# Kernel optimization log

Measured on AMD Instinct MI355X. Metric: run time of the kernel, lower is better.

The kernel has to match this reference:

```python
import jax, jax.numpy as jnp
import numpy as np

B, T, C = 2, 2048, 2048
N_HEAD, N_KV_HEAD = 16, 4
HEAD_DIM = C // N_HEAD  # 128
EPS = 1e-6


def rms_norm(x):
    # no learned scale, normalize over head_dim (last axis)
    return x * jax.lax.rsqrt(jnp.mean(jnp.square(x), axis=-1, keepdims=True) + EPS)


def apply_rotary_emb(x, cos, sin):
    # x: [B, T, H, D]; cos/sin: [T, D/2]  (rotate-half RoPE)
    x1, x2 = jnp.split(x, 2, axis=-1)
    c = cos[None, :, None, :]
    s = sin[None, :, None, :]
    return jnp.concatenate([x1 * c - x2 * s, x1 * s + x2 * c], axis=-1)


def setup_inputs() -> dict:
    key = jax.random.key(0)
    ks = jax.random.split(key, 6)
    x = jax.random.normal(ks[0], (B, T, C), dtype=jnp.float32)
    # real rotary tables: theta = 10000^{-2i/D}
    inv_freq = 1.0 / (10000.0 ** (jnp.arange(0, HEAD_DIM, 2, dtype=jnp.float32) / HEAD_DIM))
    angles = jnp.arange(T, dtype=jnp.float32)[:, None] * inv_freq[None, :]  # [T, D/2]
    cos, sin = jnp.cos(angles), jnp.sin(angles)
    std = 0.02
    Wq = jax.random.normal(ks[1], (C, N_HEAD * HEAD_DIM), dtype=jnp.float32) * std
    Wk = jax.random.normal(ks[2], (C, N_KV_HEAD * HEAD_DIM), dtype=jnp.float32) * std
    Wv = jax.random.normal(ks[3], (C, N_KV_HEAD * HEAD_DIM), dtype=jnp.float32) * std
    Wp = jax.random.normal(ks[4], (C, C), dtype=jnp.float32) * std
    return {"x": x, "cos": cos, "sin": sin, "Wq": Wq, "Wk": Wk, "Wv": Wv, "Wp": Wp}


def reference(x, cos, sin, Wq, Wk, Wv, Wp):
    Bx, Tx, Cx = x.shape
    q = (x @ Wq).reshape(Bx, Tx, N_HEAD, HEAD_DIM)
    k = (x @ Wk).reshape(Bx, Tx, N_KV_HEAD, HEAD_DIM)
    v = (x @ Wv).reshape(Bx, Tx, N_KV_HEAD, HEAD_DIM)
    q = rms_norm(apply_rotary_emb(q, cos, sin))
    k = rms_norm(apply_rotary_emb(k, cos, sin))
    # module scales q by 1/sqrt(D) AND nn.dot_product_attention scales again
    q = q * (1.0 / jnp.sqrt(HEAD_DIM))
    # GQA head repeat
    n_rep = N_HEAD // N_KV_HEAD
    k = jnp.repeat(k, n_rep, axis=2)  # [B, T, H, D]
    v = jnp.repeat(v, n_rep, axis=2)
    scores = jnp.einsum("bthd,bshd->bhts", q, k) / jnp.sqrt(jnp.asarray(HEAD_DIM, x.dtype))
    causal = jnp.tril(jnp.ones((Tx, Tx), dtype=bool))  # key <= query
    scores = jnp.where(causal[None, None, :, :], scores, jnp.finfo(scores.dtype).min)
    probs = jax.nn.softmax(scores, axis=-1)
    y = jnp.einsum("bhts,bshd->bthd", probs, v).reshape(Bx, Tx, Cx)
    return y @ Wp
```

## Files before the change

### kernel.cpp

```cpp
#include <hip/hip_runtime.h>
#include <hip/hip_bf16.h>
#include <math.h>

#define B_  2
#define T_  2048
#define C_  2048
#define NH_ 16
#define NKV_ 4
#define HD_ 128
#define NREP_ (NH_/NKV_)

#define QKVLD 3072
#define KOFF  2048
#define VOFF  2560

typedef __bf16 bf16x8 __attribute__((ext_vector_type(8)));
typedef float  f32x4  __attribute__((ext_vector_type(4)));

__device__ inline void gload_lds16(const void* g, void* l) {
    __builtin_amdgcn_global_load_lds((const __attribute__((address_space(1))) void*)g,
                                     (__attribute__((address_space(3))) void*)l, 16, 0, 0);
}

__global__ __launch_bounds__(256) void cast_bf16(const float* __restrict__ src,
                                                 __bf16* __restrict__ dst)
{
    size_t i = ((size_t)blockIdx.x * 256 + threadIdx.x) * 8;
    float4 a = *(const float4*)&src[i];
    float4 b = *(const float4*)&src[i + 4];
    union { __bf16 h[8]; uint4 u; } pk;
    pk.h[0] = (__bf16)a.x; pk.h[1] = (__bf16)a.y; pk.h[2] = (__bf16)a.z; pk.h[3] = (__bf16)a.w;
    pk.h[4] = (__bf16)b.x; pk.h[5] = (__bf16)b.y; pk.h[6] = (__bf16)b.z; pk.h[7] = (__bf16)b.w;
    *(uint4*)&dst[i] = pk.u;
}

__global__ __launch_bounds__(256) void wtrans(const float* __restrict__ src,
                                              __bf16* __restrict__ dst, int ncols)
{
    __shared__ float tl[32][33];
    int n0 = blockIdx.x * 32;
    int k0 = blockIdx.y * 32;
    int tid = threadIdx.x;
    int r  = tid >> 3;
    int c4 = (tid & 7) * 4;
    float4 v = *(const float4*)&src[(size_t)(k0 + r) * ncols + n0 + c4];
    tl[r][c4] = v.x; tl[r][c4 + 1] = v.y; tl[r][c4 + 2] = v.z; tl[r][c4 + 3] = v.w;
    __syncthreads();
    union { __bf16 h[4]; uint2 u; } pk;
#pragma unroll
    for (int j = 0; j < 4; ++j) pk.h[j] = (__bf16)tl[c4 + j][r];
    *(uint2*)&dst[(size_t)(n0 + r) * 2048 + k0 + c4] = pk.u;
}

template<typename TOUT>
__global__ __launch_bounds__(256) void gemm_bt(const __bf16* __restrict__ A,
                                               const __bf16* __restrict__ Bt,
                                               TOUT* __restrict__ C,
                                               int M, int N, int K, int ldc)
{
    __shared__ __bf16 As[128 * 32];
    __shared__ __bf16 Bs[128 * 32];

    const int tid  = threadIdx.x;
    const int wv   = tid >> 6;
    const int lane = tid & 63;
    const int grp  = lane >> 4;
    const int id16 = lane & 15;
    const int wr   = wv >> 1;
    const int wc   = wv & 1;

    const int row0 = blockIdx.y * 128;
    const int col0 = blockIdx.x * 128;

    const int sm = tid >> 2;
    const int sk = (tid & 3) << 3;

    const __bf16* ga0 = A  + (size_t)(row0 + sm) * K + sk;
    const __bf16* ga1 = A  + (size_t)(row0 + 64 + sm) * K + sk;
    const __bf16* gb0 = Bt + (size_t)(col0 + sm) * K + sk;
    const __bf16* gb1 = Bt + (size_t)(col0 + 64 + sm) * K + sk;

    __bf16* lA0 = As + (wv << 9);
    __bf16* lA1 = As + 2048 + (wv << 9);
    __bf16* lB0 = Bs + (wv << 9);
    __bf16* lB1 = Bs + 2048 + (wv << 9);

    f32x4 acc[4][4];
    const f32x4 fz = {0.f, 0.f, 0.f, 0.f};
#pragma unroll
    for (int i = 0; i < 4; ++i)
#pragma unroll
        for (int j = 0; j < 4; ++j) acc[i][j] = fz;

    for (int k0 = 0; k0 < K; k0 += 32) {
        gload_lds16(ga0 + k0, lA0);
        gload_lds16(ga1 + k0, lA1);
        gload_lds16(gb0 + k0, lB0);
        gload_lds16(gb1 + k0, lB1);
        asm volatile("s_waitcnt vmcnt(0)" ::: "memory");
        __syncthreads();

        bf16x8 af[4], bfr[4];
#pragma unroll
        for (int i = 0; i < 4; ++i)
            af[i] = *(const bf16x8*)&As[((wr << 6) + (i << 4) + id16) * 32 + (grp << 3)];
#pragma unroll
        for (int j = 0; j < 4; ++j)
            bfr[j] = *(const bf16x8*)&Bs[((wc << 6) + (j << 4) + id16) * 32 + (grp << 3)];
#pragma unroll
        for (int i = 0; i < 4; ++i)
#pragma unroll
            for (int j = 0; j < 4; ++j)
                acc[i][j] = __builtin_amdgcn_mfma_f32_16x16x32_bf16(af[i], bfr[j], acc[i][j], 0, 0, 0);
        __syncthreads();
    }

#pragma unroll
    for (int i = 0; i < 4; ++i) {
        int gr = row0 + (wr << 6) + (i << 4) + (grp << 2);
#pragma unroll
        for (int j = 0; j < 4; ++j) {
            int gc = col0 + (wc << 6) + (j << 4) + id16;
#pragma unroll
            for (int r = 0; r < 4; ++r) {
                if constexpr (sizeof(TOUT) == 4)
                    C[(size_t)(gr + r) * ldc + gc] = acc[i][j][r];
                else
                    C[(size_t)(gr + r) * ldc + gc] = (TOUT)acc[i][j][r];
            }
        }
    }
}

__global__ __launch_bounds__(256) void rope_rms_b(__bf16* __restrict__ base,
                                                  const float* __restrict__ cosb,
                                                  const float* __restrict__ sinb,
                                                  int nheads, float scale)
{
    int wid  = blockIdx.x * 4 + (threadIdx.x >> 6);
    int lane = threadIdx.x & 63;
    int bt = wid / nheads;
    int hd = wid % nheads;
    int t  = bt % T_;

    __bf16* p = base + (size_t)bt * QKVLD + hd * HD_;
    float c = cosb[t * 64 + lane];
    float s = sinb[t * 64 + lane];
    float x1 = (float)p[lane];
    float x2 = (float)p[lane + 64];
    float r1 = x1 * c - x2 * s;
    float r2 = x1 * s + x2 * c;
    float ss = r1 * r1 + r2 * r2;
#pragma unroll
    for (int off = 32; off; off >>= 1) ss += __shfl_xor(ss, off, 64);
    float inv = rsqrtf(ss * (1.f / 128.f) + 1e-6f) * scale;
    p[lane]      = (__bf16)(r1 * inv);
    p[lane + 64] = (__bf16)(r2 * inv);
}

__global__ __launch_bounds__(256) void vtrans(const __bf16* __restrict__ qkv,
                                              __bf16* __restrict__ vt)
{
    __shared__ __bf16 tl[32][HD_ + 8];
    int bx  = blockIdx.x;
    int st  = bx & 63;
    int bkv = bx >> 6;
    int b = bkv >> 2, kv = bkv & 3;
    int s0 = st << 5;
    int tid = threadIdx.x;
    {
        int s = tid >> 3;
        int d = (tid & 7) << 4;
        const __bf16* src = qkv + (size_t)(b * T_ + s0 + s) * QKVLD + VOFF + kv * HD_ + d;
        *(bf16x8*)&tl[s][d]     = *(const bf16x8*)src;
        *(bf16x8*)&tl[s][d + 8] = *(const bf16x8*)(src + 8);
    }
    __syncthreads();
    {
        int d  = tid >> 1;
        int sh = (tid & 1) << 4;
        __bf16 tmp[16];
#pragma unroll
        for (int j = 0; j < 16; ++j) tmp[j] = tl[sh + j][d];
        __bf16* dst = vt + ((size_t)(b * NKV_ + kv) * HD_ + d) * T_ + s0 + sh;
        *(bf16x8*)dst       = *(bf16x8*)&tmp[0];
        *(bf16x8*)(dst + 8) = *(bf16x8*)&tmp[8];
    }
}

#define KT2 64
#define PP  72

__global__ __launch_bounds__(256) void attn_mfma2(const __bf16* __restrict__ qkv,
                                                  const __bf16* __restrict__ vbT,
                                                  __bf16* __restrict__ y)
{
    __shared__ __bf16 Ks[2][KT2 * 128];
    __shared__ __bf16 VTs[2][128 * KT2];
    __shared__ __bf16 Ps[4][16 * PP];

    const int tid  = threadIdx.x;
    const int wv   = tid >> 6;
    const int lane = tid & 63;
    const int grp  = lane >> 4;
    const int id16 = lane & 15;

    const int bx = blockIdx.x;
    const int j  = bx & 15;
    const int bh = bx >> 4;
    const int b  = bh >> 4;
    const int h  = bh & 15;
    const int kv = h >> 2;

    const int q0a = j << 6;
    const int q0b = (31 - j) << 6;
    const int NTa = j + 1;
    const int NT  = 33;

    const int l4 = lane >> 4, l8 = lane >> 3;
    size_t koff[4], voff[4];
#pragma unroll
    for (int i = 0; i < 4; ++i) {
        int key = wv * 16 + i * 4 + l4;
        int ch  = (lane & 15) ^ (i * 4 + l4);
        koff[i] = (size_t)key * (QKVLD * 2) + ch * 16;
        int d   = wv * 32 + i * 8 + l8;
        int ch2 = (lane & 7) ^ l8;
        voff[i] = (size_t)d * (T_ * 2) + ch2 * 16;
    }
    const char* kg = (const char*)(qkv + (size_t)b * T_ * QKVLD + KOFF + kv * HD_);
    const char* vg = (const char*)(vbT + ((size_t)(b * NKV_ + kv) * HD_) * T_);

    bf16x8 qf[4], qf2[4];
    {
        const __bf16* qp = qkv + (size_t)(b * T_ + q0a + wv * 16 + id16) * QKVLD + h * HD_ + (grp << 3);
#pragma unroll
        for (int c = 0; c < 4; ++c) qf[c] = *(const bf16x8*)(qp + c * 32);
        const __bf16* qp2 = qkv + (size_t)(b * T_ + q0b + wv * 16 + id16) * QKVLD + h * HD_ + (grp << 3);
#pragma unroll
        for (int c = 0; c < 4; ++c) qf2[c] = *(const bf16x8*)(qp2 + c * 32);
    }

    const f32x4 fz = {0.f, 0.f, 0.f, 0.f};
    f32x4 o[8];
#pragma unroll
    for (int c = 0; c < 8; ++c) o[c] = fz;
    float m_r[4], l_r[4];
#pragma unroll
    for (int r = 0; r < 4; ++r) { m_r[r] = -1e30f; l_r[r] = 0.f; }

    int qbase = q0a + wv * 16;
    int q0c   = q0a;

    {
        __bf16* kl = &Ks[0][(wv * 16) * 128];
        __bf16* vl = &VTs[0][(wv * 32) * 64];
#pragma unroll
        for (int i = 0; i < 4; ++i) gload_lds16(kg + koff[i], kl + i * 4 * 128);
#pragma unroll
        for (int i = 0; i < 4; ++i) gload_lds16(vg + voff[i], vl + i * 8 * 64);
    }

    for (int tt = 0; tt < NT; ++tt) {
        const int bufc = tt & 1;
        asm volatile("s_waitcnt vmcnt(0)" ::: "memory");
        __syncthreads();

        if (tt + 1 < NT) {
            int tn = tt + 1;
            int sn = (tn >= NTa ? tn - NTa : tn) << 6;
            __bf16* kl = &Ks[tn & 1][(wv * 16) * 128];
            __bf16* vl = &VTs[tn & 1][(wv * 32) * 64];
            const char* kp = kg + (size_t)sn * (QKVLD * 2);
            const char* vp = vg + (size_t)sn * 2;
#pragma unroll
            for (int i = 0; i < 4; ++i) gload_lds16(kp + koff[i], kl + i * 4 * 128);
#pragma unroll
            for (int i = 0; i < 4; ++i) gload_lds16(vp + voff[i], vl + i * 8 * 64);
        }

        if (tt == NTa) {
            float inv[4];
#pragma unroll
            for (int r = 0; r < 4; ++r) inv[r] = 1.f / l_r[r];
#pragma unroll
            for (int r = 0; r < 4; ++r) {
                int q = qbase + (grp << 2) + r;
                __bf16* yp = y + (size_t)(b * T_ + q) * C_ + h * HD_ + id16;
#pragma unroll
                for (int c = 0; c < 8; ++c) yp[c * 16] = (__bf16)(o[c][r] * inv[r]);
            }
#pragma unroll
            for (int c = 0; c < 8; ++c) o[c] = fz;
#pragma unroll
            for (int r = 0; r < 4; ++r) { m_r[r] = -1e30f; l_r[r] = 0.f; }
#pragma unroll
            for (int c = 0; c < 4; ++c) qf[c] = qf2[c];
            qbase = q0b + wv * 16;
            q0c   = q0b;
        }

        const int s0 = (tt >= NTa ? tt - NTa : tt) << 6;

        f32x4 S[4];
#pragma unroll
        for (int t = 0; t < 4; ++t) S[t] = fz;
#pragma unroll
        for (int c = 0; c < 4; ++c) {
#pragma unroll
            for (int t = 0; t < 4; ++t) {
                bf16x8 kf = *(const bf16x8*)&Ks[bufc][(t * 16 + id16) * 128 + ((((c << 2) + grp) ^ id16) << 3)];
                S[t] = __builtin_amdgcn_mfma_f32_16x16x32_bf16(qf[c], kf, S[t], 0, 0, 0);
            }
        }
        if (s0 == q0c) {
#pragma unroll
            for (int t = 0; t < 4; ++t)
#pragma unroll
                for (int r = 0; r < 4; ++r)
                    if (s0 + t * 16 + id16 > qbase + (grp << 2) + r) S[t][r] = -1e30f;
        }

        float corr[4];
#pragma unroll
        for (int r = 0; r < 4; ++r) {
            float mx = fmaxf(fmaxf(S[0][r], S[1][r]), fmaxf(S[2][r], S[3][r]));
            mx = fmaxf(mx, __shfl_xor(mx, 1, 64));
            mx = fmaxf(mx, __shfl_xor(mx, 2, 64));
            mx = fmaxf(mx, __shfl_xor(mx, 4, 64));
            mx = fmaxf(mx, __shfl_xor(mx, 8, 64));
            float mn = fmaxf(m_r[r], mx);
            corr[r] = __expf(m_r[r] - mn);
            m_r[r]  = mn;
            float rs = 0.f;
#pragma unroll
            for (int t = 0; t < 4; ++t) {
                float p = __expf(S[t][r] - mn);
                S[t][r] = p;
                rs += p;
            }
            rs += __shfl_xor(rs, 1, 64);
            rs += __shfl_xor(rs, 2, 64);
            rs += __shfl_xor(rs, 4, 64);
            rs += __shfl_xor(rs, 8, 64);
            l_r[r] = l_r[r] * corr[r] + rs;
        }

        __bf16* pw = Ps[wv];
#pragma unroll
        for (int t = 0; t < 4; ++t)
#pragma unroll
            for (int r = 0; r < 4; ++r)
                pw[((grp << 2) + r) * PP + t * 16 + id16] = (__bf16)S[t][r];

#pragma unroll
        for (int c = 0; c < 8; ++c)
#pragma unroll
            for (int r = 0; r < 4; ++r) o[c][r] *= corr[r];

        asm volatile("s_waitcnt lgkmcnt(0)" ::: "memory");
        bf16x8 pf0 = *(const bf16x8*)&pw[id16 * PP + (grp << 3)];
        bf16x8 pf1 = *(const bf16x8*)&pw[id16 * PP + 32 + (grp << 3)];

#pragma unroll
        for (int c2 = 0; c2 < 8; ++c2) {
            bf16x8 vf0 = *(const bf16x8*)&VTs[bufc][(c2 * 16 + id16) * 64 + ((grp ^ (id16 & 7)) << 3)];
            o[c2] = __builtin_amdgcn_mfma_f32_16x16x32_bf16(pf0, vf0, o[c2], 0, 0, 0);
            bf16x8 vf1 = *(const bf16x8*)&VTs[bufc][(c2 * 16 + id16) * 64 + (((4 + grp) ^ (id16 & 7)) << 3)];
            o[c2] = __builtin_amdgcn_mfma_f32_16x16x32_bf16(pf1, vf1, o[c2], 0, 0, 0);
        }
    }

    {
        float inv[4];
#pragma unroll
        for (int r = 0; r < 4; ++r) inv[r] = 1.f / l_r[r];
#pragma unroll
        for (int r = 0; r < 4; ++r) {
            int q = qbase + (grp << 2) + r;
            __bf16* yp = y + (size_t)(b * T_ + q) * C_ + h * HD_ + id16;
#pragma unroll
            for (int c = 0; c < 8; ++c) yp[c * 16] = (__bf16)(o[c][r] * inv[r]);
        }
    }
}

extern "C" void kernel_launch(void* const* d_in, const int* in_sizes, int n_in,
                              void* d_out, int out_size, void* d_ws, size_t ws_size,
                              hipStream_t stream)
{
    const float* x    = (const float*)d_in[0];
    const float* cosb = (const float*)d_in[1];
    const float* sinb = (const float*)d_in[2];
    const float* Wq   = (const float*)d_in[3];
    const float* Wk   = (const float*)d_in[4];
    const float* Wv   = (const float*)d_in[5];
    const float* Wp   = (const float*)d_in[6];
    float* out = (float*)d_out;

    const int M = B_ * T_;

    char* w = (char*)d_ws;
    __bf16* xb    = (__bf16*)w;  w += (size_t)M * C_ * 2;
    __bf16* qkv   = (__bf16*)w;  w += (size_t)M * QKVLD * 2;
    __bf16* wqkvT = (__bf16*)w;  w += (size_t)QKVLD * C_ * 2;
    __bf16* wpT   = (__bf16*)w;  w += (size_t)C_ * C_ * 2;
    __bf16* vt    = (__bf16*)w;  w += (size_t)M * NKV_ * HD_ * 2;
    __bf16* y     = (__bf16*)w;

    cast_bf16<<<(M * C_) / 2048, 256, 0, stream>>>(x, xb);
    wtrans<<<dim3(C_ / 32, C_ / 32), 256, 0, stream>>>(Wq, wqkvT, C_);
    wtrans<<<dim3(512 / 32, C_ / 32), 256, 0, stream>>>(Wk, wqkvT + (size_t)KOFF * C_, 512);
    wtrans<<<dim3(512 / 32, C_ / 32), 256, 0, stream>>>(Wv, wqkvT + (size_t)VOFF * C_, 512);
    wtrans<<<dim3(C_ / 32, C_ / 32), 256, 0, stream>>>(Wp, wpT, C_);

    gemm_bt<__bf16><<<dim3(QKVLD / 128, M / 128), 256, 0, stream>>>(xb, wqkvT, qkv, M, QKVLD, C_, QKVLD);

    rope_rms_b<<<(M * NH_) / 4, 256, 0, stream>>>(qkv, cosb, sinb, NH_, 0.0078125f);
    rope_rms_b<<<(M * NKV_) / 4, 256, 0, stream>>>(qkv + KOFF, cosb, sinb, NKV_, 1.0f);

    vtrans<<<B_ * NKV_ * (T_ / 32), 256, 0, stream>>>(qkv, vt);

    attn_mfma2<<<B_ * NH_ * 16, 256, 0, stream>>>(qkv, vt, y);

    gemm_bt<float><<<dim3(C_ / 128, M / 128), 256, 0, stream>>>(y, wpT, out, M, C_, C_, C_);
}
```

Baseline: 356.5 us.

## Drop online-softmax max tracking, double-buffer GEMM LDS, fuse QKV weight transposes

Because q and k are RMS-normalized, the scaled scores are bounded, so attention drops the running max and rescaling. It folds log2(e) into the q scale and uses exp2, deferring the row-sum reduction to the end. The GEMM kernel now double-buffers its LDS tiles, so the next tile's global loads overlap the current MFMAs and one barrier per step is removed. The three QKV weight-transpose launches are merged into one. The max-free softmax relies on the normalization bound holding, and double buffering doubles GEMM LDS use.

```diff
diff --git a/kernel.cpp b/kernel.cpp
--- a/kernel.cpp
+++ b/kernel.cpp
@@ -14,6 +14,8 @@
 #define KOFF  2048
 #define VOFF  2560
 
+#define QSCALE 0.01127105500694502f
+
 typedef __bf16 bf16x8 __attribute__((ext_vector_type(8)));
 typedef float  f32x4  __attribute__((ext_vector_type(4)));
 
@@ -32,6 +34,32 @@
     pk.h[0] = (__bf16)a.x; pk.h[1] = (__bf16)a.y; pk.h[2] = (__bf16)a.z; pk.h[3] = (__bf16)a.w;
     pk.h[4] = (__bf16)b.x; pk.h[5] = (__bf16)b.y; pk.h[6] = (__bf16)b.z; pk.h[7] = (__bf16)b.w;
     *(uint4*)&dst[i] = pk.u;
+}
+
+__global__ __launch_bounds__(256) void wtrans_qkv(const float* __restrict__ Wq,
+                                                  const float* __restrict__ Wk,
+                                                  const float* __restrict__ Wv,
+                                                  __bf16* __restrict__ dst)
+{
+    __shared__ float tl[32][33];
+    int ct = blockIdx.x;
+    int k0 = blockIdx.y * 32;
+    const float* src;
+    int ncols, c0, dr0;
+    if (ct < 64)      { src = Wq; ncols = 2048; c0 = ct * 32;        dr0 = ct * 32; }
+    else if (ct < 80) { src = Wk; ncols = 512;  c0 = (ct - 64) * 32; dr0 = KOFF + (ct - 64) * 32; }
+    else              { src = Wv; ncols = 512;  c0 = (ct - 80) * 32; dr0 = VOFF + (ct - 80) * 32; }
+
+    int tid = threadIdx.x;
+    int r  = tid >> 3;
+    int c4 = (tid & 7) * 4;
+    float4 v = *(const float4*)&src[(size_t)(k0 + r) * ncols + c0 + c4];
+    tl[r][c4] = v.x; tl[r][c4 + 1] = v.y; tl[r][c4 + 2] = v.z; tl[r][c4 + 3] = v.w;
+    __syncthreads();
+    union { __bf16 h[4]; uint2 u; } pk;
+#pragma unroll
+    for (int j = 0; j < 4; ++j) pk.h[j] = (__bf16)tl[c4 + j][r];
+    *(uint2*)&dst[(size_t)(dr0 + r) * 2048 + k0 + c4] = pk.u;
 }
 
 __global__ __launch_bounds__(256) void wtrans(const float* __restrict__ src,
@@ -58,8 +86,8 @@
                                                TOUT* __restrict__ C,
                                                int M, int N, int K, int ldc)
 {
-    __shared__ __bf16 As[128 * 32];
-    __shared__ __bf16 Bs[128 * 32];
+    __shared__ __bf16 As[2][128 * 32];
+    __shared__ __bf16 Bs[2][128 * 32];
 
     const int tid  = threadIdx.x;
     const int wv   = tid >> 6;
@@ -80,11 +108,6 @@
     const __bf16* gb0 = Bt + (size_t)(col0 + sm) * K + sk;
     const __bf16* gb1 = Bt + (size_t)(col0 + 64 + sm) * K + sk;
 
-    __bf16* lA0 = As + (wv << 9);
-    __bf16* lA1 = As + 2048 + (wv << 9);
-    __bf16* lB0 = Bs + (wv << 9);
-    __bf16* lB1 = Bs + 2048 + (wv << 9);
-
     f32x4 acc[4][4];
     const f32x4 fz = {0.f, 0.f, 0.f, 0.f};
 #pragma unroll
@@ -92,27 +115,44 @@
 #pragma unroll
         for (int j = 0; j < 4; ++j) acc[i][j] = fz;
 
-    for (int k0 = 0; k0 < K; k0 += 32) {
-        gload_lds16(ga0 + k0, lA0);
-        gload_lds16(ga1 + k0, lA1);
-        gload_lds16(gb0 + k0, lB0);
-        gload_lds16(gb1 + k0, lB1);
+    const int nk = K >> 5;
+
+    {
+        __bf16* a0 = &As[0][wv << 9];
+        __bf16* b0 = &Bs[0][wv << 9];
+        gload_lds16(ga0, a0);
+        gload_lds16(ga1, a0 + 2048);
+        gload_lds16(gb0, b0);
+        gload_lds16(gb1, b0 + 2048);
+    }
+
+    for (int kt = 0; kt < nk; ++kt) {
+        const int bufc = kt & 1;
         asm volatile("s_waitcnt vmcnt(0)" ::: "memory");
         __syncthreads();
 
+        if (kt + 1 < nk) {
+            const int kb = (kt + 1) << 5;
+            __bf16* a0 = &As[1 - bufc][wv << 9];
+            __bf16* b0 = &Bs[1 - bufc][wv << 9];
+            gload_lds16(ga0 + kb, a0);
+            gload_lds16(ga1 + kb, a0 + 2048);
+            gload_lds16(gb0 + kb, b0);
+            gload_lds16(gb1 + kb, b0 + 2048);
+        }
+
         bf16x8 af[4], bfr[4];
 #pragma unroll
         for (int i = 0; i < 4; ++i)
-            af[i] = *(const bf16x8*)&As[((wr << 6) + (i << 4) + id16) * 32 + (grp << 3)];
+            af[i] = *(const bf16x8*)&As[bufc][((wr << 6) + (i << 4) + id16) * 32 + (grp << 3)];
 #pragma unroll
         for (int j = 0; j < 4; ++j)
-            bfr[j] = *(const bf16x8*)&Bs[((wc << 6) + (j << 4) + id16) * 32 + (grp << 3)];
+            bfr[j] = *(const bf16x8*)&Bs[bufc][((wc << 6) + (j << 4) + id16) * 32 + (grp << 3)];
 #pragma unroll
         for (int i = 0; i < 4; ++i)
 #pragma unroll
             for (int j = 0; j < 4; ++j)
                 acc[i][j] = __builtin_amdgcn_mfma_f32_16x16x32_bf16(af[i], bfr[j], acc[i][j], 0, 0, 0);
-        __syncthreads();
     }
 
 #pragma unroll
@@ -245,9 +285,9 @@
     f32x4 o[8];
 #pragma unroll
     for (int c = 0; c < 8; ++c) o[c] = fz;
-    float m_r[4], l_r[4];
-#pragma unroll
-    for (int r = 0; r < 4; ++r) { m_r[r] = -1e30f; l_r[r] = 0.f; }
+    float l_r[4];
+#pragma unroll
+    for (int r = 0; r < 4; ++r) l_r[r] = 0.f;
 
     int qbase = q0a + wv * 16;
     int q0c   = q0a;
@@ -282,7 +322,14 @@
         if (tt == NTa) {
             float inv[4];
 #pragma unroll
-            for (int r = 0; r < 4; ++r) inv[r] = 1.f / l_r[r];
+            for (int r = 0; r < 4; ++r) {
+                float l = l_r[r];
+                l += __shfl_xor(l, 1, 64);
+                l += __shfl_xor(l, 2, 64);
+                l += __shfl_xor(l, 4, 64);
+                l += __shfl_xor(l, 8, 64);
+                inv[r] = 1.f / l;
+            }
 #pragma unroll
             for (int r = 0; r < 4; ++r) {
                 int q = qbase + (grp << 2) + r;
@@ -293,7 +340,7 @@
 #pragma unroll
             for (int c = 0; c < 8; ++c) o[c] = fz;
 #pragma unroll
-            for (int r = 0; r < 4; ++r) { m_r[r] = -1e30f; l_r[r] = 0.f; }
+            for (int r = 0; r < 4; ++r) l_r[r] = 0.f;
 #pragma unroll
             for (int c = 0; c < 4; ++c) qf[c] = qf2[c];
             qbase = q0b + wv * 16;
@@ -321,30 +368,13 @@
                     if (s0 + t * 16 + id16 > qbase + (grp << 2) + r) S[t][r] = -1e30f;
         }
 
-        float corr[4];
-#pragma unroll
-        for (int r = 0; r < 4; ++r) {
-            float mx = fmaxf(fmaxf(S[0][r], S[1][r]), fmaxf(S[2][r], S[3][r]));
-            mx = fmaxf(mx, __shfl_xor(mx, 1, 64));
-            mx = fmaxf(mx, __shfl_xor(mx, 2, 64));
-            mx = fmaxf(mx, __shfl_xor(mx, 4, 64));
-            mx = fmaxf(mx, __shfl_xor(mx, 8, 64));
-            float mn = fmaxf(m_r[r], mx);
-            corr[r] = __expf(m_r[r] - mn);
-            m_r[r]  = mn;
-            float rs = 0.f;
-#pragma unroll
-            for (int t = 0; t < 4; ++t) {
-                float p = __expf(S[t][r] - mn);
-                S[t][r] = p;
-                rs += p;
-            }
-            rs += __shfl_xor(rs, 1, 64);
-            rs += __shfl_xor(rs, 2, 64);
-            rs += __shfl_xor(rs, 4, 64);
-            rs += __shfl_xor(rs, 8, 64);
-            l_r[r] = l_r[r] * corr[r] + rs;
-        }
+#pragma unroll
+        for (int t = 0; t < 4; ++t)
+#pragma unroll
+            for (int r = 0; r < 4; ++r) S[t][r] = exp2f(S[t][r]);
+#pragma unroll
+        for (int r = 0; r < 4; ++r)
+            l_r[r] += (S[0][r] + S[1][r]) + (S[2][r] + S[3][r]);
 
         __bf16* pw = Ps[wv];
 #pragma unroll
@@ -352,11 +382,6 @@
 #pragma unroll
             for (int r = 0; r < 4; ++r)
                 pw[((grp << 2) + r) * PP + t * 16 + id16] = (__bf16)S[t][r];
-
-#pragma unroll
-        for (int c = 0; c < 8; ++c)
-#pragma unroll
-            for (int r = 0; r < 4; ++r) o[c][r] *= corr[r];
 
         asm volatile("s_waitcnt lgkmcnt(0)" ::: "memory");
         bf16x8 pf0 = *(const bf16x8*)&pw[id16 * PP + (grp << 3)];
@@ -374,7 +399,14 @@
     {
         float inv[4];
 #pragma unroll
-        for (int r = 0; r < 4; ++r) inv[r] = 1.f / l_r[r];
+        for (int r = 0; r < 4; ++r) {
+            float l = l_r[r];
+            l += __shfl_xor(l, 1, 64);
+            l += __shfl_xor(l, 2, 64);
+            l += __shfl_xor(l, 4, 64);
+            l += __shfl_xor(l, 8, 64);
+            inv[r] = 1.f / l;
+        }
 #pragma unroll
         for (int r = 0; r < 4; ++r) {
             int q = qbase + (grp << 2) + r;
@@ -409,14 +441,12 @@
     __bf16* y     = (__bf16*)w;
 
     cast_bf16<<<(M * C_) / 2048, 256, 0, stream>>>(x, xb);
-    wtrans<<<dim3(C_ / 32, C_ / 32), 256, 0, stream>>>(Wq, wqkvT, C_);
-    wtrans<<<dim3(512 / 32, C_ / 32), 256, 0, stream>>>(Wk, wqkvT + (size_t)KOFF * C_, 512);
-    wtrans<<<dim3(512 / 32, C_ / 32), 256, 0, stream>>>(Wv, wqkvT + (size_t)VOFF * C_, 512);
+    wtrans_qkv<<<dim3(96, C_ / 32), 256, 0, stream>>>(Wq, Wk, Wv, wqkvT);
     wtrans<<<dim3(C_ / 32, C_ / 32), 256, 0, stream>>>(Wp, wpT, C_);
 
     gemm_bt<__bf16><<<dim3(QKVLD / 128, M / 128), 256, 0, stream>>>(xb, wqkvT, qkv, M, QKVLD, C_, QKVLD);
 
-    rope_rms_b<<<(M * NH_) / 4, 256, 0, stream>>>(qkv, cosb, sinb, NH_, 0.0078125f);
+    rope_rms_b<<<(M * NH_) / 4, 256, 0, stream>>>(qkv, cosb, sinb, NH_, QSCALE);
     rope_rms_b<<<(M * NKV_) / 4, 256, 0, stream>>>(qkv + KOFF, cosb, sinb, NKV_, 1.0f);
 
     vtrans<<<B_ * NKV_ * (T_ / 32), 256, 0, stream>>>(qkv, vt);
```

Result: faster. 320.9 us (-10.0%).
